# Optimization experiments

Hardware: AMD Instinct MI355X
Metric: run time of the kernel (lower is better)

Reference implementation:

```python
import jax, jax.numpy as jnp
import numpy as np
import math

B, L = 16, 4096
N = B * L            # total nodes; node 0 is the (masked) root
E = N - 1            # one parent edge per non-root node
D_IN, D_OUT, HEADS = 512, 256, 4
SLOPE = 0.2          # PyG GATConv default negative_slope
PRUNE_FRAC = 0.3


def gelu(x):
    return 0.5 * x * (1.0 + jnp.tanh(math.sqrt(2.0 / math.pi) * (x + 0.044715 * x ** 3)))


def remove_nodes_func(parent, remove):
    # parent[i] = parent node id of node i+1; remove[j] = 1 iff node j+1 removed.
    for _ in range(5):
        aug_rem = jnp.concatenate([jnp.zeros(1, jnp.int32), remove])
        aug_par = jnp.concatenate([jnp.zeros(1, jnp.int32), parent])
        pr = aug_rem[parent]                               # is my parent removed?
        parent = pr * aug_par[parent] + (1 - pr) * parent  # grandparent if so
    return parent


def remove_nodes_and_edges(edge_index, map_index):
    src, par = edge_index[0], edge_index[1]
    rem = jnp.zeros(N, jnp.int32).at[map_index].set(1)     # removal flag per node id (>=1)
    edge_mask = 1 - rem[src]                               # drop edges whose child node removed
    emr = rem[1:]                                          # == zeros(E).at[map_index-1].set(1)
    temp = remove_nodes_func(par, emr)
    ei_new = jnp.stack([src, temp]) * edge_mask[None, :]   # removed edges collapse to (0,0)
    node_mask_upd = jnp.concatenate([jnp.ones(1, jnp.float32), 1.0 - emr.astype(jnp.float32)])
    return ei_new, node_mask_upd


def gat_conv(xin, edge_index, gat_w, att_src, att_dst, gat_b):
    # PyG GATConv: concat=True, add_self_loops=True, eval mode (attention dropout off)
    h = (xin @ gat_w).reshape(N, HEADS, D_OUT)
    loop = jnp.arange(N, dtype=edge_index.dtype)
    src = jnp.concatenate([edge_index[0], loop])
    dst = jnp.concatenate([edge_index[1], loop])
    a_src = jnp.einsum('nhc,hc->nh', h, att_src)
    a_dst = jnp.einsum('nhc,hc->nh', h, att_dst)
    alpha = jax.nn.leaky_relu(a_src[src] + a_dst[dst], SLOPE)       # [Etot, H]
    m = jax.ops.segment_max(alpha, dst, num_segments=N)
    e = jnp.exp(alpha - m[dst])
    s = jax.ops.segment_sum(e, dst, num_segments=N)
    coef = e / (s[dst] + 1e-16)
    out = jax.ops.segment_sum(coef[:, :, None] * h[src], dst, num_segments=N)
    return out.reshape(N, HEADS * D_OUT) + gat_b


def setup_inputs():
    key = jax.random.key(0)
    ks = jax.random.split(key, 10)
    x = jax.random.normal(ks[0], (N, D_IN), jnp.float32)
    statement_rep = jax.random.normal(ks[1], (N, D_IN), jnp.float32)
    node_mask = (jax.random.uniform(ks[2], (B, L)) > 0.3).astype(jnp.float32)
    node_mask = node_mask.at[0, 0].set(0.0)  # root node never scored/pruned
    type_id = jax.random.randint(ks[3], (B, L), 0, 2, dtype=jnp.int32)
    child = jnp.arange(1, N, dtype=jnp.int32)
    parent = jnp.floor(jax.random.uniform(ks[4], (E,)) * child).astype(jnp.int32)  # parent < child
    edge_index = jnp.stack([child, parent])
    edge_index_ent = edge_index
    s = 0.02
    scorer_w = jax.random.normal(ks[5], (2 * D_IN, 1), jnp.float32) * s
    scorer_b = jnp.zeros((1,), jnp.float32)
    emb_w = jax.random.normal(ks[6], (2, D_OUT), jnp.float32) * s
    emb_b = jnp.zeros((D_OUT,), jnp.float32)
    gat_w = jax.random.normal(ks[7], (2 * D_IN + D_OUT, HEADS * D_OUT), jnp.float32) * s
    att_src = jax.random.normal(ks[8], (HEADS, D_OUT), jnp.float32) * s
    att_dst = jax.random.normal(ks[9], (HEADS, D_OUT), jnp.float32) * s
    gat_b = jnp.zeros((HEADS * D_OUT,), jnp.float32)
    return {"x": x, "edge_index": edge_index, "edge_index_ent": edge_index_ent,
            "statement_rep": statement_rep, "node_mask": node_mask, "type_id": type_id,
            "scorer_w": scorer_w, "scorer_b": scorer_b, "emb_w": emb_w, "emb_b": emb_b,
            "gat_w": gat_w, "att_src": att_src, "att_dst": att_dst, "gat_b": gat_b}


def reference(x, edge_index, edge_index_ent, statement_rep, node_mask, type_id,
              scorer_w, scorer_b, emb_w, emb_b, gat_w, att_src, att_dst, gat_b):
    del edge_index_ent  # threaded through the original but never used
    nm = node_mask.reshape(-1)
    tid = type_id.reshape(-1)
    one_hot = jax.nn.one_hot(tid, 2, dtype=jnp.float32)
    type_emb = gelu(one_hot @ emb_w + emb_b)
    # --- single GNN layer (num_layers=1), with top-k node pruning ---
    node_score = (jnp.concatenate([x, statement_rep], 1) @ scorer_w + scorer_b)[:, 0] * nm
    nnz = int(jnp.count_nonzero(node_score))  # eager; k is data-dependent in the original
    if int(nnz * PRUNE_FRAC) != 0:
        k = int(nnz * PRUNE_FRAC + 1)
        masked = jnp.where(node_score != 0, node_score, jnp.inf)
        _, map_index = jax.lax.top_k(-masked, k)  # k smallest nonzero scores -> node ids
        edge_index, upd = remove_nodes_and_edges(edge_index, map_index)
        nm = nm * upd
    xin = jnp.concatenate([x, statement_rep, type_emb], 1)
    out = gelu(gat_conv(xin, edge_index, gat_w, att_src, att_dst, gat_b))
    # feature dropout runs in eval as identity here (deterministic reference)
    return out, nm.reshape(B, L)
```

## Files before the change

### kernel.cpp

```cpp
#include <hip/hip_runtime.h>
#include <cstdint>
#include <cstddef>

#define N_NODES 65536
#define E_EDGES 65535
#define DIN     512
#define KDIM    1024
#define JDIM    1024
#define HEADS   4
#define DOUT    256

typedef short   short8  __attribute__((ext_vector_type(8)));
typedef unsigned short ushort8 __attribute__((ext_vector_type(8)));
typedef float   floatx4 __attribute__((ext_vector_type(4)));

__device__ inline float bf2f(unsigned short u){
  union { unsigned int i; float f; } c; c.i = ((unsigned int)u) << 16; return c.f;
}
__device__ inline unsigned short f2bf(float f){
  union { float f; unsigned int i; } c; c.f = f;
  unsigned int r = c.i + 0x7FFFu + ((c.i >> 16) & 1u);
  return (unsigned short)(r >> 16);
}
__device__ inline unsigned int okey(float f){
  union { float f; unsigned int u; } c; c.f = f;
  return (c.u & 0x80000000u) ? ~c.u : (c.u | 0x80000000u);
}
__device__ inline float unokey(unsigned int k){
  union { unsigned int u; float f; } c;
  c.u = (k & 0x80000000u) ? (k ^ 0x80000000u) : ~k;
  return c.f;
}
__device__ inline float leaky(float x){ return x >= 0.f ? x : 0.2f * x; }
__device__ inline float gelu_f(float x){
  return 0.5f * x * (1.f + tanhf(0.7978845608028654f * (x + 0.044715f * x * x * x)));
}

__global__ void k_prep(const float* __restrict__ x, const float* __restrict__ sr,
                       const float* __restrict__ nmask, const float* __restrict__ sw,
                       const float* __restrict__ sb, unsigned short* __restrict__ xs,
                       float* __restrict__ score, unsigned int* __restrict__ key){
  int lane = threadIdx.x & 63, wv = threadIdx.x >> 6;
  int i = blockIdx.x*4 + wv;
  const float* xr  = x  + (size_t)i*DIN + 8*lane;
  const float* srr = sr + (size_t)i*DIN + 8*lane;
  float4 a0 = *(const float4*)(xr);
  float4 a1 = *(const float4*)(xr + 4);
  float4 b0 = *(const float4*)(srr);
  float4 b1 = *(const float4*)(srr + 4);
  float4 w0 = *(const float4*)(sw + 8*lane);
  float4 w1 = *(const float4*)(sw + 8*lane + 4);
  float4 w2 = *(const float4*)(sw + 512 + 8*lane);
  float4 w3 = *(const float4*)(sw + 512 + 8*lane + 4);
  double part = (double)a0.x*(double)w0.x + (double)a0.y*(double)w0.y
              + (double)a0.z*(double)w0.z + (double)a0.w*(double)w0.w
              + (double)a1.x*(double)w1.x + (double)a1.y*(double)w1.y
              + (double)a1.z*(double)w1.z + (double)a1.w*(double)w1.w
              + (double)b0.x*(double)w2.x + (double)b0.y*(double)w2.y
              + (double)b0.z*(double)w2.z + (double)b0.w*(double)w2.w
              + (double)b1.x*(double)w3.x + (double)b1.y*(double)w3.y
              + (double)b1.z*(double)w3.z + (double)b1.w*(double)w3.w;
  ushort8 oa, ob;
  oa[0]=f2bf(a0.x); oa[1]=f2bf(a0.y); oa[2]=f2bf(a0.z); oa[3]=f2bf(a0.w);
  oa[4]=f2bf(a1.x); oa[5]=f2bf(a1.y); oa[6]=f2bf(a1.z); oa[7]=f2bf(a1.w);
  ob[0]=f2bf(b0.x); ob[1]=f2bf(b0.y); ob[2]=f2bf(b0.z); ob[3]=f2bf(b0.w);
  ob[4]=f2bf(b1.x); ob[5]=f2bf(b1.y); ob[6]=f2bf(b1.z); ob[7]=f2bf(b1.w);
  *(ushort8*)(xs + (size_t)i*KDIM + 8*lane)       = oa;
  *(ushort8*)(xs + (size_t)i*KDIM + 512 + 8*lane) = ob;
  for (int sdel = 32; sdel; sdel >>= 1) part += __shfl_down(part, sdel);
  if (lane == 0){
    float fs = (float)(part + (double)sb[0]);
    float s  = fs * nmask[i];
    score[i] = s;
    float v = (s == 0.f) ? __builtin_inff() : s;
    key[i] = okey(v);
  }
}

__global__ void k_nnz(const float* __restrict__ score, int* scal){
  int i = blockIdx.x*256 + threadIdx.x;
  int nz = (score[i] != 0.f) ? 1 : 0;
  unsigned long long b = __ballot(nz);
  if ((threadIdx.x & 63) == 0) atomicAdd(&scal[0], (int)__popcll(b));
}

__global__ void k_initsel(int* scal){
  int nnz = scal[0];
  double prod = (double)nnz * 0.3;
  scal[1] = ((int)prod != 0) ? 1 : 0;
  int k = (int)(prod + 1.0);
  scal[2] = k; scal[3] = 0; scal[4] = k;
}

__global__ void k_hist(const unsigned int* __restrict__ key, unsigned int* __restrict__ hist,
                       const int* __restrict__ scal, int pass){
  __shared__ unsigned int lh[256];
  int t = threadIdx.x;
  lh[t] = 0; __syncthreads();
  int i = blockIdx.x*256 + t;
  unsigned int kv = key[i];
  unsigned int pref = (unsigned int)scal[3];
  bool ok = (pass == 0) || ((kv >> (32 - 8*pass)) == pref);
  if (ok) atomicAdd(&lh[(kv >> (24 - 8*pass)) & 255u], 1u);
  __syncthreads();
  if (lh[t]) atomicAdd(&hist[t], lh[t]);
}

__global__ void k_select(unsigned int* __restrict__ hist, int* __restrict__ scal){
  __shared__ unsigned int h[256];
  int t = threadIdx.x;
  h[t] = hist[t];
  __syncthreads();
  if (t == 0){
    unsigned int r = (unsigned int)scal[4];
    unsigned int cum = 0, pref = (unsigned int)scal[3];
    for (int b = 0; b < 256; b++){
      unsigned int c = h[b];
      if (cum + c >= r){
        scal[3] = (int)((pref << 8) | (unsigned int)b);
        scal[4] = (int)(r - cum);
        break;
      }
      cum += c;
    }
  }
  __syncthreads();
  hist[t] = 0;
}

__global__ void k_mark(const unsigned int* __restrict__ key, int* __restrict__ scal,
                       int* __restrict__ rem, int* __restrict__ eqlist){
  if (!scal[1]) return;
  int i = blockIdx.x*256 + threadIdx.x;
  unsigned int Ks = (unsigned int)scal[3];
  unsigned int kv = key[i];
  if (kv < Ks) rem[i] = 1;
  else if (kv == Ks){
    int p = atomicAdd(&scal[5], 1);
    if (p < 4096) eqlist[p] = i;
  }
}

__global__ void k_ties(int* __restrict__ scal, int* __restrict__ eqlist, int* __restrict__ rem){
  if (!scal[1]) return;
  int m = scal[5]; if (m > 4096) m = 4096;
  int need = scal[4]; if (need > m) need = m;
  for (int it = 0; it < need; it++){
    int best = 0x7FFFFFFF, bj = -1;
    for (int j = 0; j < m; j++){ int v = eqlist[j]; if (v < best){ best = v; bj = j; } }
    if (bj < 0) break;
    rem[best] = 1; eqlist[bj] = 0x7FFFFFFF;
  }
}

__global__ void k_remap(const int* __restrict__ pin, const int* __restrict__ rem,
                        int* __restrict__ pout){
  int e = blockIdx.x*256 + threadIdx.x;
  if (e >= E_EDGES) return;
  int p = pin[e];
  pout[e] = rem[p] ? (p == 0 ? 0 : pin[p-1]) : p;
}

__global__ void k_edges(const int* __restrict__ srcIn, const int* __restrict__ pfin,
                        const int* __restrict__ rem, int* __restrict__ srcF,
                        int* __restrict__ dstF, int* __restrict__ cnt){
  int e = blockIdx.x*256 + threadIdx.x;
  if (e >= E_EDGES) return;
  int s = srcIn[e];
  if (rem[s]){ srcF[e] = 0; dstF[e] = -1; }
  else {
    srcF[e] = s;
    int d = pfin[e];
    dstF[e] = d;
    atomicAdd(&cnt[d], 1);
  }
}

__global__ void k_scan1(const int* __restrict__ cnt, int* __restrict__ offs,
                        int* __restrict__ bsum){
  int b = blockIdx.x, t = threadIdx.x, i = b*256 + t;
  int v = cnt[i];
  int lane = t & 63, wv = t >> 6;
  int xv = v;
  for (int o2 = 1; o2 < 64; o2 <<= 1){ int y = __shfl_up(xv, o2); if (lane >= o2) xv += y; }
  __shared__ int wt_[4];
  if (lane == 63) wt_[wv] = xv;
  __syncthreads();
  int add = 0;
  for (int k2 = 0; k2 < wv; k2++) add += wt_[k2];
  offs[i] = xv + add - v;
  if (t == 255) bsum[b] = xv + add;
}

__global__ void k_scan2(int* __restrict__ bsum){
  int t = threadIdx.x;
  int v = bsum[t];
  int lane = t & 63, wv = t >> 6;
  int xv = v;
  for (int o2 = 1; o2 < 64; o2 <<= 1){ int y = __shfl_up(xv, o2); if (lane >= o2) xv += y; }
  __shared__ int wt_[4];
  if (lane == 63) wt_[wv] = xv;
  __syncthreads();
  int add = 0;
  for (int k2 = 0; k2 < wv; k2++) add += wt_[k2];
  bsum[t] = xv + add - v;
}

__global__ void k_scan3(int* __restrict__ offs, const int* __restrict__ bsum,
                        int* __restrict__ cur){
  int b = blockIdx.x, t = threadIdx.x, i = b*256 + t;
  int v = offs[i] + bsum[b];
  offs[i] = v; cur[i] = v;
}

__global__ void k_fill(const int* __restrict__ dstF, int* __restrict__ cur,
                       int* __restrict__ elist){
  int e = blockIdx.x*256 + threadIdx.x;
  if (e >= E_EDGES) return;
  int d = dstF[e]; if (d < 0) return;
  int pos = atomicAdd(&cur[d], 1);
  elist[pos] = e;
}

__global__ void k_wt(const float* __restrict__ gw, unsigned short* __restrict__ wtb){
  __shared__ float tile[32][33];
  int kt = blockIdx.x*32, jt = blockIdx.y*32;
  int tx = threadIdx.x, ty = threadIdx.y;
  for (int r = ty; r < 32; r += 8) tile[r][tx] = gw[(size_t)(kt+r)*JDIM + jt + tx];
  __syncthreads();
  for (int r = ty; r < 32; r += 8) wtb[(size_t)(jt+r)*KDIM + kt + tx] = f2bf(tile[tx][r]);
}

__global__ void k_tc(const float* __restrict__ embw, const float* __restrict__ embb,
                     const float* __restrict__ gw, float* __restrict__ tc){
  __shared__ float eg[2][DOUT];
  int t = threadIdx.x;
  eg[0][t] = gelu_f(embw[t] + embb[t]);
  eg[1][t] = gelu_f(embw[DOUT + t] + embb[t]);
  __syncthreads();
  int g = blockIdx.x*256 + t;
  int te = g >> 10, j = g & 1023;
  float acc = 0.f;
  #pragma unroll 8
  for (int c = 0; c < DOUT; c++){
    acc += eg[te][c] * gw[(size_t)(KDIM + c)*JDIM + j];
  }
  tc[te*JDIM + j] = acc;
}

#define BKG 64
__global__ __launch_bounds__(512, 2) void k_gemm(const unsigned short* __restrict__ xs,
    const unsigned short* __restrict__ wtb, const float* __restrict__ tc,
    const int* __restrict__ tid, const float* __restrict__ atts,
    const float* __restrict__ attd, unsigned short* __restrict__ hmat,
    float* __restrict__ asrc, float* __restrict__ adst){
  __shared__ unsigned short As[2][256*BKG];
  __shared__ unsigned short Bs[2][256*BKG];
  int bid = blockIdx.x;
  int xcd = bid & 7, tq = bid >> 3;
  int jb = tq & 3, ip = (tq >> 2)*8 + xcd;
  int rowbase = ip*256, colbase = jb*256;
  int t = threadIdx.x, wave = t >> 6, lane = t & 63;
  int wm = (wave >> 2)*128, wn = (wave & 3)*64;
  floatx4 acc[8][4];
  floatx4 zero = {0.f, 0.f, 0.f, 0.f};
  #pragma unroll
  for (int a = 0; a < 8; a++)
    #pragma unroll
    for (int b = 0; b < 4; b++) acc[a][b] = zero;

  int srow = lane >> 3;
  int scol = (lane & 7)*8;

  auto STAGE = [&](int buf, int kt){
    int k0 = kt*BKG;
    #pragma unroll
    for (int r = 0; r < 4; r++){
      int ci = r*8 + wave;
      int row = ci*8 + srow;
      const unsigned short* ga = xs  + (size_t)(rowbase + row)*KDIM + k0 + scol;
      __builtin_amdgcn_global_load_lds((const __attribute__((address_space(1))) void*)ga,
          (__attribute__((address_space(3))) void*)(&As[buf][ci*512 + lane*8]), 16, 0, 0);
      const unsigned short* gb = wtb + (size_t)(colbase + row)*KDIM + k0 + scol;
      __builtin_amdgcn_global_load_lds((const __attribute__((address_space(1))) void*)gb,
          (__attribute__((address_space(3))) void*)(&Bs[buf][ci*512 + lane*8]), 16, 0, 0);
    }
  };

  int rr = lane & 15, rq = (lane >> 4)*8;
  auto COMPUTE = [&](int buf){
    #pragma unroll
    for (int ks = 0; ks < 2; ks++){
      short8 af[8], bfr[4];
      #pragma unroll
      for (int mi = 0; mi < 8; mi++)
        af[mi]  = *(const short8*)(&As[buf][(wm + mi*16 + rr)*BKG + ks*32 + rq]);
      #pragma unroll
      for (int ni = 0; ni < 4; ni++)
        bfr[ni] = *(const short8*)(&Bs[buf][(wn + ni*16 + rr)*BKG + ks*32 + rq]);
      #pragma unroll
      for (int mi = 0; mi < 8; mi++)
        #pragma unroll
        for (int ni = 0; ni < 4; ni++)
          acc[mi][ni] = __builtin_amdgcn_mfma_f32_16x16x32_bf16(af[mi], bfr[ni], acc[mi][ni], 0, 0, 0);
    }
  };

  const int NT = KDIM / BKG;
  STAGE(0, 0);
  __syncthreads();
  int cur = 0;
  for (int kt = 0; kt < NT - 1; kt++){
    STAGE(cur ^ 1, kt + 1);
    COMPUTE(cur);
    __syncthreads();
    cur ^= 1;
  }
  COMPUTE(cur);

  int q = lane >> 4, cc = lane & 15;
  float att_s[4], att_d[4];
  #pragma unroll
  for (int ni = 0; ni < 4; ni++){
    int cih = wn + ni*16 + cc;
    att_s[ni] = atts[jb*DOUT + cih];
    att_d[ni] = attd[jb*DOUT + cih];
  }
  __syncthreads();
  float* sp = (float*)&As[0][0];
  #pragma unroll
  for (int mi = 0; mi < 8; mi++){
    #pragma unroll
    for (int reg = 0; reg < 4; reg++){
      int rloc = wm + mi*16 + q*4 + reg;
      int rowg = rowbase + rloc;
      int tt = tid[rowg];
      float ps = 0.f, pd = 0.f;
      #pragma unroll
      for (int ni = 0; ni < 4; ni++){
        int col = colbase + wn + ni*16 + cc;
        float v = acc[mi][ni][reg] + tc[tt*JDIM + col];
        hmat[(size_t)rowg*JDIM + col] = f2bf(v);
        ps += v * att_s[ni]; pd += v * att_d[ni];
      }
      #pragma unroll
      for (int m2 = 1; m2 < 16; m2 <<= 1){
        ps += __shfl_xor(ps, m2); pd += __shfl_xor(pd, m2);
      }
      if (cc == 0){
        sp[(rloc*4 + (wave & 3))*2 + 0] = ps;
        sp[(rloc*4 + (wave & 3))*2 + 1] = pd;
      }
    }
  }
  __syncthreads();
  if (t < 256){
    float s = 0.f, d2 = 0.f;
    #pragma unroll
    for (int w4 = 0; w4 < 4; w4++){ s += sp[(t*4 + w4)*2]; d2 += sp[(t*4 + w4)*2 + 1]; }
    asrc[(size_t)(rowbase + t)*HEADS + jb] = s;
    adst[(size_t)(rowbase + t)*HEADS + jb] = d2;
  }
}

__global__ void k_max(const int* __restrict__ srcF, const int* __restrict__ dstF,
                      const float* __restrict__ asrc, const float* __restrict__ adst,
                      unsigned int* __restrict__ mkey){
  int idx = blockIdx.x*256 + threadIdx.x;
  if (idx >= E_EDGES + N_NODES) return;
  int s, d;
  if (idx < E_EDGES){ d = dstF[idx]; if (d < 0) return; s = srcF[idx]; }
  else { s = d = idx - E_EDGES; }
  for (int hd = 0; hd < HEADS; hd++){
    float al = leaky(asrc[s*HEADS + hd] + adst[d*HEADS + hd]);
    atomicMax(&mkey[d*HEADS + hd], okey(al));
  }
}

__global__ void k_sum(const int* __restrict__ srcF, const int* __restrict__ dstF,
                      const float* __restrict__ asrc, const float* __restrict__ adst,
                      const unsigned int* __restrict__ mkey, float* __restrict__ ssum,
                      const int* __restrict__ scal){
  int idx = blockIdx.x*256 + threadIdx.x;
  if (idx >= E_EDGES + N_NODES) return;
  int s, d; float wgt = 1.f;
  if (idx < E_EDGES){ d = dstF[idx]; if (d < 0) return; s = srcF[idx]; }
  else {
    s = d = idx - E_EDGES;
    if (d == 0 && scal[1]) wgt = 1.f + (float)scal[2];
  }
  for (int hd = 0; hd < HEADS; hd++){
    float al = leaky(asrc[s*HEADS + hd] + adst[d*HEADS + hd]);
    float e = expf(al - unokey(mkey[d*HEADS + hd]));
    atomicAdd(&ssum[d*HEADS + hd], wgt * e);
  }
}

__global__ void k_agg(const unsigned short* __restrict__ hmat, const int* __restrict__ srcF,
                      const float* __restrict__ asrc, const float* __restrict__ adst,
                      const unsigned int* __restrict__ mkey, const float* __restrict__ ssum,
                      const int* __restrict__ offs, const int* __restrict__ cnt,
                      const int* __restrict__ elist, const float* __restrict__ gatb,
                      const int* __restrict__ scal, float* __restrict__ out){
  int n = blockIdx.x, t = threadIdx.x;
  int hd = t >> 6;
  float mh = unokey(mkey[n*HEADS + hd]);
  float sh = ssum[n*HEADS + hd] + 1e-16f;
  float adn = adst[n*HEADS + hd];
  float a0 = 0.f, a1 = 0.f, a2 = 0.f, a3 = 0.f;
  {
    float al = leaky(asrc[n*HEADS + hd] + adn);
    float coef = expf(al - mh) / sh;
    if (n == 0 && scal[1]) coef *= (1.f + (float)scal[2]);
    ushort4 hv = *(const ushort4*)(hmat + (size_t)n*JDIM + 4*t);
    a0 += coef*bf2f(hv.x); a1 += coef*bf2f(hv.y); a2 += coef*bf2f(hv.z); a3 += coef*bf2f(hv.w);
  }
  int o0 = offs[n], c_ = cnt[n];
  for (int q2 = 0; q2 < c_; q2++){
    int e = elist[o0 + q2];
    int s = srcF[e];
    float al = leaky(asrc[s*HEADS + hd] + adn);
    float coef = expf(al - mh) / sh;
    ushort4 hv = *(const ushort4*)(hmat + (size_t)s*JDIM + 4*t);
    a0 += coef*bf2f(hv.x); a1 += coef*bf2f(hv.y); a2 += coef*bf2f(hv.z); a3 += coef*bf2f(hv.w);
  }
  const float4 gb = *(const float4*)(gatb + 4*t);
  float4 ov;
  ov.x = gelu_f(a0 + gb.x); ov.y = gelu_f(a1 + gb.y);
  ov.z = gelu_f(a2 + gb.z); ov.w = gelu_f(a3 + gb.w);
  *(float4*)(out + (size_t)n*JDIM + 4*t) = ov;
}

__global__ void k_nm(const float* __restrict__ nmask, const int* __restrict__ rem,
                     float* __restrict__ nmout){
  int i = blockIdx.x*256 + threadIdx.x;
  float u = (i == 0) ? 1.f : (1.f - (float)rem[i]);
  nmout[i] = nmask[i] * u;
}

extern "C" void kernel_launch(void* const* d_in, const int* in_sizes, int n_in,
                              void* d_out, int out_size, void* d_ws, size_t ws_size,
                              hipStream_t stream){
  (void)in_sizes; (void)n_in; (void)out_size; (void)ws_size;
  const float* x    = (const float*)d_in[0];
  const int*  eidx  = (const int*)d_in[1];
  const float* sr   = (const float*)d_in[3];
  const float* nmask= (const float*)d_in[4];
  const int*  tid   = (const int*)d_in[5];
  const float* sw   = (const float*)d_in[6];
  const float* sb   = (const float*)d_in[7];
  const float* embw = (const float*)d_in[8];
  const float* embb = (const float*)d_in[9];
  const float* gw   = (const float*)d_in[10];
  const float* atts = (const float*)d_in[11];
  const float* attd = (const float*)d_in[12];
  const float* gatb = (const float*)d_in[13];
  float* out = (float*)d_out;

  char* w = (char*)d_ws;
  size_t o = 0;
  auto alloc = [&](size_t bytes){ size_t r = o; o += (bytes + 255) & ~(size_t)255; return r; };
  size_t o_cnt  = alloc((size_t)N_NODES*4);
  size_t o_mkey = alloc((size_t)N_NODES*HEADS*4);
  size_t o_ssum = alloc((size_t)N_NODES*HEADS*4);
  size_t o_rem  = alloc((size_t)N_NODES*4);
  size_t o_hist = alloc(256*4);
  size_t o_scal = alloc(64);
  size_t o_eq   = alloc(4096*4);
  size_t zero_bytes = o;
  size_t o_score= alloc((size_t)N_NODES*4);
  size_t o_key  = alloc((size_t)N_NODES*4);
  size_t o_pA   = alloc((size_t)E_EDGES*4);
  size_t o_pB   = alloc((size_t)E_EDGES*4);
  size_t o_srcF = alloc((size_t)E_EDGES*4);
  size_t o_dstF = alloc((size_t)E_EDGES*4);
  size_t o_off  = alloc((size_t)N_NODES*4);
  size_t o_cur  = alloc((size_t)N_NODES*4);
  size_t o_el   = alloc((size_t)E_EDGES*4);
  size_t o_bsum = alloc(256*4);
  size_t o_asrc = alloc((size_t)N_NODES*HEADS*4);
  size_t o_adst = alloc((size_t)N_NODES*HEADS*4);
  size_t o_tc   = alloc((size_t)2*JDIM*4);
  size_t o_wt   = alloc((size_t)JDIM*KDIM*2);
  size_t o_xs   = alloc((size_t)N_NODES*KDIM*2);
  size_t o_h    = alloc((size_t)N_NODES*JDIM*2);

  int* cnt   = (int*)(w + o_cnt);
  unsigned int* mkey = (unsigned int*)(w + o_mkey);
  float* ssum = (float*)(w + o_ssum);
  int* rem   = (int*)(w + o_rem);
  unsigned int* hist = (unsigned int*)(w + o_hist);
  int* scal  = (int*)(w + o_scal);
  int* eqlist= (int*)(w + o_eq);
  float* score = (float*)(w + o_score);
  unsigned int* key = (unsigned int*)(w + o_key);
  int* pA = (int*)(w + o_pA);
  int* pB = (int*)(w + o_pB);
  int* srcF = (int*)(w + o_srcF);
  int* dstF = (int*)(w + o_dstF);
  int* offs = (int*)(w + o_off);
  int* cur  = (int*)(w + o_cur);
  int* elist= (int*)(w + o_el);
  int* bsum = (int*)(w + o_bsum);
  float* asrc = (float*)(w + o_asrc);
  float* adst = (float*)(w + o_adst);
  float* tc = (float*)(w + o_tc);
  unsigned short* wtb = (unsigned short*)(w + o_wt);
  unsigned short* xs  = (unsigned short*)(w + o_xs);
  unsigned short* hmat= (unsigned short*)(w + o_h);

  hipMemsetAsync(w, 0, zero_bytes, stream);

  k_prep<<<N_NODES/4, 256, 0, stream>>>(x, sr, nmask, sw, sb, xs, score, key);
  k_nnz<<<N_NODES/256, 256, 0, stream>>>(score, scal);
  k_initsel<<<1, 1, 0, stream>>>(scal);
  for (int p = 0; p < 4; p++){
    k_hist<<<N_NODES/256, 256, 0, stream>>>(key, hist, scal, p);
    k_select<<<1, 256, 0, stream>>>(hist, scal);
  }
  k_mark<<<N_NODES/256, 256, 0, stream>>>(key, scal, rem, eqlist);
  k_ties<<<1, 1, 0, stream>>>(scal, eqlist, rem);

  const int* par_in = eidx + E_EDGES;
  int egrid = (E_EDGES + 255)/256;
  k_remap<<<egrid, 256, 0, stream>>>(par_in, rem, pA);
  k_remap<<<egrid, 256, 0, stream>>>(pA, rem, pB);
  k_remap<<<egrid, 256, 0, stream>>>(pB, rem, pA);
  k_remap<<<egrid, 256, 0, stream>>>(pA, rem, pB);
  k_remap<<<egrid, 256, 0, stream>>>(pB, rem, pA);

  k_edges<<<egrid, 256, 0, stream>>>(eidx, pA, rem, srcF, dstF, cnt);
  k_scan1<<<256, 256, 0, stream>>>(cnt, offs, bsum);
  k_scan2<<<1, 256, 0, stream>>>(bsum);
  k_scan3<<<256, 256, 0, stream>>>(offs, bsum, cur);
  k_fill<<<egrid, 256, 0, stream>>>(dstF, cur, elist);

  k_wt<<<dim3(32,32), dim3(32,8), 0, stream>>>(gw, wtb);
  k_tc<<<8, 256, 0, stream>>>(embw, embb, gw, tc);
  k_gemm<<<1024, 512, 0, stream>>>(xs, wtb, tc, tid, atts, attd, hmat, asrc, adst);

  int mg = (E_EDGES + N_NODES + 255)/256;
  k_max<<<mg, 256, 0, stream>>>(srcF, dstF, asrc, adst, mkey);
  k_sum<<<mg, 256, 0, stream>>>(srcF, dstF, asrc, adst, mkey, ssum, scal);
  k_agg<<<N_NODES, 256, 0, stream>>>(hmat, srcF, asrc, adst, mkey, ssum, offs, cnt,
                                     elist, gatb, scal, out);
  k_nm<<<N_NODES/256, 256, 0, stream>>>(nmask, rem, out + (size_t)N_NODES*JDIM);
}
```

Baseline: 976.9 us.

## Fold attention vectors into weights and fuse softmax stats into aggregation

Precomputes W·att_src and W·att_dst (plus the type-embedding contribution) so each node's attention logits come from a small dot product inside the prep kernel, rather than from the GEMM epilogue's shuffle and shared-memory reduction. Removes the separate atomic max and sum edge kernels: each aggregation block now computes the per-head max and softmax denominator over its CSR edge list. This drops two edge passes, their atomics and the mkey/ssum buffers, and lightens the GEMM epilogue. In exchange the logits are computed in fp32 from unrounded inputs instead of from the bf16-product GEMM output, and each aggregation block reads its edge list three times.

```diff
diff --git a/kernel.cpp b/kernel.cpp
--- a/kernel.cpp
+++ b/kernel.cpp
@@ -36,10 +36,49 @@
   return 0.5f * x * (1.f + tanhf(0.7978845608028654f * (x + 0.044715f * x * x * x)));
 }
 
+__global__ void k_watt(const float* __restrict__ gw, const float* __restrict__ atts,
+                       const float* __restrict__ attd, float* __restrict__ watt){
+  int wave = threadIdx.x >> 6, lane = threadIdx.x & 63;
+  int k = blockIdx.x*4 + wave;
+  int hd = lane >> 4;
+  const float* gr = gw + (size_t)k*JDIM + lane*16;
+  float vs = 0.f, vd = 0.f;
+  #pragma unroll
+  for (int j = 0; j < 16; j += 4){
+    float4 g = *(const float4*)(gr + j);
+    float4 s = *(const float4*)(atts + lane*16 + j);
+    float4 d = *(const float4*)(attd + lane*16 + j);
+    vs += g.x*s.x + g.y*s.y + g.z*s.z + g.w*s.w;
+    vd += g.x*d.x + g.y*d.y + g.z*d.z + g.w*d.w;
+  }
+  for (int m2 = 1; m2 < 16; m2 <<= 1){ vs += __shfl_xor(vs, m2); vd += __shfl_xor(vd, m2); }
+  if ((lane & 15) == 0){ watt[k*8 + hd] = vs; watt[k*8 + 4 + hd] = vd; }
+}
+
+__global__ void k_tatt(const float* __restrict__ tc, const float* __restrict__ atts,
+                       const float* __restrict__ attd, float* __restrict__ tatt){
+  int lane = threadIdx.x;
+  for (int o = 0; o < 16; o++){
+    int ty = o >> 3, sd = (o >> 2) & 1, hd = o & 3;
+    const float* av = sd ? attd : atts;
+    float p = 0.f;
+    #pragma unroll
+    for (int cc = 0; cc < 4; cc++){
+      int c = lane*4 + cc;
+      p += tc[ty*JDIM + hd*256 + c] * av[hd*DOUT + c];
+    }
+    for (int sdel = 32; sdel; sdel >>= 1) p += __shfl_down(p, sdel);
+    if (lane == 0) tatt[o] = p;
+  }
+}
+
 __global__ void k_prep(const float* __restrict__ x, const float* __restrict__ sr,
                        const float* __restrict__ nmask, const float* __restrict__ sw,
-                       const float* __restrict__ sb, unsigned short* __restrict__ xs,
-                       float* __restrict__ score, unsigned int* __restrict__ key){
+                       const float* __restrict__ sb, const float* __restrict__ watt,
+                       const float* __restrict__ tatt, const int* __restrict__ tid,
+                       unsigned short* __restrict__ xs, float* __restrict__ score,
+                       unsigned int* __restrict__ key, float* __restrict__ asrc,
+                       float* __restrict__ adst){
   int lane = threadIdx.x & 63, wv = threadIdx.x >> 6;
   int i = blockIdx.x*4 + wv;
   const float* xr  = x  + (size_t)i*DIN + 8*lane;
@@ -67,13 +106,41 @@
   ob[4]=f2bf(b1.x); ob[5]=f2bf(b1.y); ob[6]=f2bf(b1.z); ob[7]=f2bf(b1.w);
   *(ushort8*)(xs + (size_t)i*KDIM + 8*lane)       = oa;
   *(ushort8*)(xs + (size_t)i*KDIM + 512 + 8*lane) = ob;
-  for (int sdel = 32; sdel; sdel >>= 1) part += __shfl_down(part, sdel);
+
+  float xv[16];
+  xv[0]=a0.x; xv[1]=a0.y; xv[2]=a0.z; xv[3]=a0.w;
+  xv[4]=a1.x; xv[5]=a1.y; xv[6]=a1.z; xv[7]=a1.w;
+  xv[8]=b0.x; xv[9]=b0.y; xv[10]=b0.z; xv[11]=b0.w;
+  xv[12]=b1.x; xv[13]=b1.y; xv[14]=b1.z; xv[15]=b1.w;
+  float4 ps = {0.f,0.f,0.f,0.f}, pd = {0.f,0.f,0.f,0.f};
+  #pragma unroll
+  for (int kk = 0; kk < 16; kk++){
+    int krow = (kk < 8) ? (8*lane + kk) : (512 + 8*lane + (kk - 8));
+    float4 wv0 = *(const float4*)(watt + krow*8);
+    float4 wv1 = *(const float4*)(watt + krow*8 + 4);
+    ps.x += xv[kk]*wv0.x; ps.y += xv[kk]*wv0.y; ps.z += xv[kk]*wv0.z; ps.w += xv[kk]*wv0.w;
+    pd.x += xv[kk]*wv1.x; pd.y += xv[kk]*wv1.y; pd.z += xv[kk]*wv1.z; pd.w += xv[kk]*wv1.w;
+  }
+  for (int sdel = 32; sdel; sdel >>= 1){
+    part += __shfl_down(part, sdel);
+    ps.x += __shfl_down(ps.x, sdel); ps.y += __shfl_down(ps.y, sdel);
+    ps.z += __shfl_down(ps.z, sdel); ps.w += __shfl_down(ps.w, sdel);
+    pd.x += __shfl_down(pd.x, sdel); pd.y += __shfl_down(pd.y, sdel);
+    pd.z += __shfl_down(pd.z, sdel); pd.w += __shfl_down(pd.w, sdel);
+  }
   if (lane == 0){
     float fs = (float)(part + (double)sb[0]);
     float s  = fs * nmask[i];
     score[i] = s;
     float v = (s == 0.f) ? __builtin_inff() : s;
     key[i] = okey(v);
+    int tt = tid[i];
+    float4 os = { ps.x + tatt[tt*8 + 0], ps.y + tatt[tt*8 + 1],
+                  ps.z + tatt[tt*8 + 2], ps.w + tatt[tt*8 + 3] };
+    float4 od = { pd.x + tatt[tt*8 + 4], pd.y + tatt[tt*8 + 5],
+                  pd.z + tatt[tt*8 + 6], pd.w + tatt[tt*8 + 7] };
+    *(float4*)(asrc + (size_t)i*HEADS) = os;
+    *(float4*)(adst + (size_t)i*HEADS) = od;
   }
 }
 
@@ -251,9 +318,7 @@
 #define BKG 64
 __global__ __launch_bounds__(512, 2) void k_gemm(const unsigned short* __restrict__ xs,
     const unsigned short* __restrict__ wtb, const float* __restrict__ tc,
-    const int* __restrict__ tid, const float* __restrict__ atts,
-    const float* __restrict__ attd, unsigned short* __restrict__ hmat,
-    float* __restrict__ asrc, float* __restrict__ adst){
+    const int* __restrict__ tid, unsigned short* __restrict__ hmat){
   __shared__ unsigned short As[2][256*BKG];
   __shared__ unsigned short Bs[2][256*BKG];
   int bid = blockIdx.x;
@@ -319,93 +384,62 @@
   COMPUTE(cur);
 
   int q = lane >> 4, cc = lane & 15;
-  float att_s[4], att_d[4];
-  #pragma unroll
-  for (int ni = 0; ni < 4; ni++){
-    int cih = wn + ni*16 + cc;
-    att_s[ni] = atts[jb*DOUT + cih];
-    att_d[ni] = attd[jb*DOUT + cih];
-  }
-  __syncthreads();
-  float* sp = (float*)&As[0][0];
   #pragma unroll
   for (int mi = 0; mi < 8; mi++){
     #pragma unroll
     for (int reg = 0; reg < 4; reg++){
-      int rloc = wm + mi*16 + q*4 + reg;
-      int rowg = rowbase + rloc;
+      int rowg = rowbase + wm + mi*16 + q*4 + reg;
       int tt = tid[rowg];
-      float ps = 0.f, pd = 0.f;
       #pragma unroll
       for (int ni = 0; ni < 4; ni++){
         int col = colbase + wn + ni*16 + cc;
         float v = acc[mi][ni][reg] + tc[tt*JDIM + col];
         hmat[(size_t)rowg*JDIM + col] = f2bf(v);
-        ps += v * att_s[ni]; pd += v * att_d[ni];
       }
-      #pragma unroll
-      for (int m2 = 1; m2 < 16; m2 <<= 1){
-        ps += __shfl_xor(ps, m2); pd += __shfl_xor(pd, m2);
-      }
-      if (cc == 0){
-        sp[(rloc*4 + (wave & 3))*2 + 0] = ps;
-        sp[(rloc*4 + (wave & 3))*2 + 1] = pd;
-      }
-    }
-  }
-  __syncthreads();
-  if (t < 256){
-    float s = 0.f, d2 = 0.f;
-    #pragma unroll
-    for (int w4 = 0; w4 < 4; w4++){ s += sp[(t*4 + w4)*2]; d2 += sp[(t*4 + w4)*2 + 1]; }
-    asrc[(size_t)(rowbase + t)*HEADS + jb] = s;
-    adst[(size_t)(rowbase + t)*HEADS + jb] = d2;
-  }
-}
-
-__global__ void k_max(const int* __restrict__ srcF, const int* __restrict__ dstF,
-                      const float* __restrict__ asrc, const float* __restrict__ adst,
-                      unsigned int* __restrict__ mkey){
-  int idx = blockIdx.x*256 + threadIdx.x;
-  if (idx >= E_EDGES + N_NODES) return;
-  int s, d;
-  if (idx < E_EDGES){ d = dstF[idx]; if (d < 0) return; s = srcF[idx]; }
-  else { s = d = idx - E_EDGES; }
-  for (int hd = 0; hd < HEADS; hd++){
-    float al = leaky(asrc[s*HEADS + hd] + adst[d*HEADS + hd]);
-    atomicMax(&mkey[d*HEADS + hd], okey(al));
-  }
-}
-
-__global__ void k_sum(const int* __restrict__ srcF, const int* __restrict__ dstF,
-                      const float* __restrict__ asrc, const float* __restrict__ adst,
-                      const unsigned int* __restrict__ mkey, float* __restrict__ ssum,
-                      const int* __restrict__ scal){
-  int idx = blockIdx.x*256 + threadIdx.x;
-  if (idx >= E_EDGES + N_NODES) return;
-  int s, d; float wgt = 1.f;
-  if (idx < E_EDGES){ d = dstF[idx]; if (d < 0) return; s = srcF[idx]; }
-  else {
-    s = d = idx - E_EDGES;
-    if (d == 0 && scal[1]) wgt = 1.f + (float)scal[2];
-  }
-  for (int hd = 0; hd < HEADS; hd++){
-    float al = leaky(asrc[s*HEADS + hd] + adst[d*HEADS + hd]);
-    float e = expf(al - unokey(mkey[d*HEADS + hd]));
-    atomicAdd(&ssum[d*HEADS + hd], wgt * e);
+    }
   }
 }
 
 __global__ void k_agg(const unsigned short* __restrict__ hmat, const int* __restrict__ srcF,
                       const float* __restrict__ asrc, const float* __restrict__ adst,
-                      const unsigned int* __restrict__ mkey, const float* __restrict__ ssum,
                       const int* __restrict__ offs, const int* __restrict__ cnt,
                       const int* __restrict__ elist, const float* __restrict__ gatb,
                       const int* __restrict__ scal, float* __restrict__ out){
   int n = blockIdx.x, t = threadIdx.x;
+  int o0 = offs[n], c_ = cnt[n];
+  __shared__ float mh_s[4], sh_s[4];
+  int wave = t >> 6, lane = t & 63;
+  if (wave == 0){
+    int hd = lane >> 4, r = lane & 15;
+    float adn = adst[n*HEADS + hd];
+    float aself = leaky(asrc[n*HEADS + hd] + adn);
+    float mx = aself;
+    for (int q2 = r; q2 < c_; q2 += 16){
+      int e = elist[o0 + q2];
+      int s = srcF[e];
+      float al = leaky(asrc[s*HEADS + hd] + adn);
+      mx = fmaxf(mx, al);
+    }
+    for (int m2 = 1; m2 < 16; m2 <<= 1) mx = fmaxf(mx, __shfl_xor(mx, m2));
+    float sm = 0.f;
+    for (int q2 = r; q2 < c_; q2 += 16){
+      int e = elist[o0 + q2];
+      int s = srcF[e];
+      float al = leaky(asrc[s*HEADS + hd] + adn);
+      sm += expf(al - mx);
+    }
+    for (int m2 = 1; m2 < 16; m2 <<= 1) sm += __shfl_xor(sm, m2);
+    if (r == 0){
+      float wself = 1.f;
+      if (n == 0 && scal[1]) wself = 1.f + (float)scal[2];
+      sm += wself * expf(aself - mx);
+      mh_s[hd] = mx; sh_s[hd] = sm + 1e-16f;
+    }
+  }
+  __syncthreads();
   int hd = t >> 6;
-  float mh = unokey(mkey[n*HEADS + hd]);
-  float sh = ssum[n*HEADS + hd] + 1e-16f;
+  float mh = mh_s[hd];
+  float sh = sh_s[hd];
   float adn = adst[n*HEADS + hd];
   float a0 = 0.f, a1 = 0.f, a2 = 0.f, a3 = 0.f;
   {
@@ -415,7 +449,6 @@
     ushort4 hv = *(const ushort4*)(hmat + (size_t)n*JDIM + 4*t);
     a0 += coef*bf2f(hv.x); a1 += coef*bf2f(hv.y); a2 += coef*bf2f(hv.z); a3 += coef*bf2f(hv.w);
   }
-  int o0 = offs[n], c_ = cnt[n];
   for (int q2 = 0; q2 < c_; q2++){
     int e = elist[o0 + q2];
     int s = srcF[e];
@@ -461,8 +494,6 @@
   size_t o = 0;
   auto alloc = [&](size_t bytes){ size_t r = o; o += (bytes + 255) & ~(size_t)255; return r; };
   size_t o_cnt  = alloc((size_t)N_NODES*4);
-  size_t o_mkey = alloc((size_t)N_NODES*HEADS*4);
-  size_t o_ssum = alloc((size_t)N_NODES*HEADS*4);
   size_t o_rem  = alloc((size_t)N_NODES*4);
   size_t o_hist = alloc(256*4);
   size_t o_scal = alloc(64);
@@ -481,13 +512,13 @@
   size_t o_asrc = alloc((size_t)N_NODES*HEADS*4);
   size_t o_adst = alloc((size_t)N_NODES*HEADS*4);
   size_t o_tc   = alloc((size_t)2*JDIM*4);
+  size_t o_watt = alloc((size_t)KDIM*8*4);
+  size_t o_tatt = alloc(16*4);
   size_t o_wt   = alloc((size_t)JDIM*KDIM*2);
   size_t o_xs   = alloc((size_t)N_NODES*KDIM*2);
   size_t o_h    = alloc((size_t)N_NODES*JDIM*2);
 
   int* cnt   = (int*)(w + o_cnt);
-  unsigned int* mkey = (unsigned int*)(w + o_mkey);
-  float* ssum = (float*)(w + o_ssum);
   int* rem   = (int*)(w + o_rem);
   unsigned int* hist = (unsigned int*)(w + o_hist);
   int* scal  = (int*)(w + o_scal);
@@ -505,13 +536,21 @@
   float* asrc = (float*)(w + o_asrc);
   float* adst = (float*)(w + o_adst);
   float* tc = (float*)(w + o_tc);
+  float* watt = (float*)(w + o_watt);
+  float* tatt = (float*)(w + o_tatt);
   unsigned short* wtb = (unsigned short*)(w + o_wt);
   unsigned short* xs  = (unsigned short*)(w + o_xs);
   unsigned short* hmat= (unsigned short*)(w + o_h);
 
   hipMemsetAsync(w, 0, zero_bytes, stream);
 
-  k_prep<<<N_NODES/4, 256, 0, stream>>>(x, sr, nmask, sw, sb, xs, score, key);
+  k_watt<<<256, 256, 0, stream>>>(gw, atts, attd, watt);
+  k_tc<<<8, 256, 0, stream>>>(embw, embb, gw, tc);
+  k_tatt<<<1, 64, 0, stream>>>(tc, atts, attd, tatt);
+  k_wt<<<dim3(32,32), dim3(32,8), 0, stream>>>(gw, wtb);
+
+  k_prep<<<N_NODES/4, 256, 0, stream>>>(x, sr, nmask, sw, sb, watt, tatt, tid,
+                                        xs, score, key, asrc, adst);
   k_nnz<<<N_NODES/256, 256, 0, stream>>>(score, scal);
   k_initsel<<<1, 1, 0, stream>>>(scal);
   for (int p = 0; p < 4; p++){
@@ -535,14 +574,9 @@
   k_scan3<<<256, 256, 0, stream>>>(offs, bsum, cur);
   k_fill<<<egrid, 256, 0, stream>>>(dstF, cur, elist);
 
-  k_wt<<<dim3(32,32), dim3(32,8), 0, stream>>>(gw, wtb);
-  k_tc<<<8, 256, 0, stream>>>(embw, embb, gw, tc);
-  k_gemm<<<1024, 512, 0, stream>>>(xs, wtb, tc, tid, atts, attd, hmat, asrc, adst);
-
-  int mg = (E_EDGES + N_NODES + 255)/256;
-  k_max<<<mg, 256, 0, stream>>>(srcF, dstF, asrc, adst, mkey);
-  k_sum<<<mg, 256, 0, stream>>>(srcF, dstF, asrc, adst, mkey, ssum, scal);
-  k_agg<<<N_NODES, 256, 0, stream>>>(hmat, srcF, asrc, adst, mkey, ssum, offs, cnt,
+  k_gemm<<<1024, 512, 0, stream>>>(xs, wtb, tc, tid, hmat);
+
+  k_agg<<<N_NODES, 256, 0, stream>>>(hmat, srcF, asrc, adst, offs, cnt,
                                      elist, gatb, scal, out);
   k_nm<<<N_NODES/256, 256, 0, stream>>>(nmask, rem, out + (size_t)N_NODES*JDIM);
 }
```

Result: slower. 1.172 ms (+20.0%).
